# Kernel tuning notes

Hardware: AMD Instinct MI355X
Metric: run time of the kernel (lower is better)

Reference implementation:

```python
import jax, jax.numpy as jnp
import numpy as np
from jax import lax

B, C, H, W = 8, 384, 64, 64


def cos_map(N):
    # ortho DCT-II basis: weight[n, x] = cos(n*(x+0.5)*pi/N) * sqrt(2/N), row 0 /= sqrt(2)
    wx = (jnp.arange(N, dtype=jnp.float32) + 0.5) / N
    wn = jnp.arange(N, dtype=jnp.float32)[:, None]
    w = jnp.cos(wn * wx[None, :] * jnp.pi) * np.sqrt(2.0 / N).astype(np.float32)
    return w.at[0, :].multiply(np.float32(1.0 / np.sqrt(2.0)))


def setup_inputs() -> dict:
    key = jax.random.key(0)
    ks = jax.random.split(key, 8)
    s = 0.05
    return {
        "x": jax.random.normal(ks[0], (B, C, H, W), jnp.float32),
        "freq_embed": jax.random.normal(ks[1], (H, W, C), jnp.float32),
        "dw_w": jax.random.normal(ks[2], (C, 1, 3, 3), jnp.float32) * s,
        "dw_b": jnp.zeros((C,), jnp.float32),
        "lin_w": jax.random.normal(ks[3], (2 * C, C), jnp.float32) * s,
        "lin_b": jnp.zeros((2 * C,), jnp.float32),
        "tok_w": jax.random.normal(ks[4], (C, C), jnp.float32) * s,
        "tok_b": jnp.zeros((C,), jnp.float32),
        "c": jnp.ones((1,), jnp.float32),
        "alpha": jnp.ones((1,), jnp.float32) * 0.1,
        "ln_g": jnp.ones((C,), jnp.float32),
        "ln_b": jnp.zeros((C,), jnp.float32),
        "out_w": jax.random.normal(ks[5], (C, C), jnp.float32) * s,
        "out_b": jnp.zeros((C,), jnp.float32),
    }


def reference(x, freq_embed, dw_w, dw_b, lin_w, lin_b, tok_w, tok_b, c, alpha, ln_g, ln_b, out_w, out_b):
    Bc, Cc, Hc, Wc = x.shape
    # depthwise 3x3 conv
    x = lax.conv_general_dilated(x, dw_w, (1, 1), 'SAME',
                                 feature_group_count=Cc,
                                 dimension_numbers=('NCHW', 'OIHW', 'NCHW'))
    x = x + dw_b[None, :, None, None]
    # linear to 2C (channels-last), split into signal x and gate z
    xz = jnp.einsum('bchw,dc->bhwd', x, lin_w) + lin_b
    xs, z = xz[..., :Cc], xz[..., Cc:]          # [B,H,W,C]
    xs = jnp.transpose(xs, (0, 3, 1, 2))        # [B,C,H,W]
    # 2D ortho DCT-II: D = Wh @ x @ Ww^T
    Wh, Ww = cos_map(Hc), cos_map(Wc)
    Xd = jnp.einsum('nh,bchw,kw->bcnk', Wh, xs, Ww)
    # learned frequency gating: t = ReLU(Linear(freq_embed)), per (H,W,C)
    t = jax.nn.relu(jnp.einsum('hwc,dc->hwd', freq_embed, tok_w) + tok_b)
    ct = jnp.transpose(jnp.cos(c * t), (2, 0, 1))[None]        # [1,C,H,W]
    st = jnp.transpose(jnp.sin(c * t), (2, 0, 1))[None] / c[0]
    # x_u0 == x_v0 == Xd in the original (dct2d applied twice to same x)
    final = ct * Xd + st * (Xd + 0.5 * alpha[0] * Xd)
    # 2D inverse DCT: x = Wh^T @ D @ Ww
    xi = jnp.einsum('nh,bcnk,kw->bchw', Wh, final, Ww)
    # LayerNorm over channels, gate with SiLU(z), output linear
    y = jnp.transpose(xi, (0, 2, 3, 1))          # [B,H,W,C]
    mu = jnp.mean(y, axis=-1, keepdims=True)
    var = jnp.mean((y - mu) ** 2, axis=-1, keepdims=True)
    y = (y - mu) * lax.rsqrt(var + 1e-5) * ln_g + ln_b
    y = y * jax.nn.silu(z)
    y = jnp.einsum('bhwc,dc->bhwd', y, out_w) + out_b
    return jnp.transpose(y, (0, 3, 1, 2))        # [B,C,H,W]
```

## Files before the change

### kernel.cpp

```cpp
#include <hip/hip_runtime.h>

typedef _Float16 h2 __attribute__((ext_vector_type(2)));
typedef _Float16 h4 __attribute__((ext_vector_type(4)));
typedef _Float16 h8 __attribute__((ext_vector_type(8)));
typedef float    f4 __attribute__((ext_vector_type(4)));

#define MFMA32(a,b,c) __builtin_amdgcn_mfma_f32_16x16x32_f16((a),(b),(c),0,0,0)
#define MFMA16(a,b,c) __builtin_amdgcn_mfma_f32_16x16x16f16((a),(b),(c),0,0,0)

#define B_N 8
#define C_N 384
#define P_N 4096
#define PI_F 3.14159265358979323846f

__device__ __forceinline__ h4 to_h4(f4 v) {
  h4 r; r[0]=(_Float16)v[0]; r[1]=(_Float16)v[1]; r[2]=(_Float16)v[2]; r[3]=(_Float16)v[3];
  return r;
}

__device__ __forceinline__ void gl_lds16(const _Float16* g, _Float16* l) {
  __builtin_amdgcn_global_load_lds(
      (const __attribute__((address_space(1))) void*)g,
      (__attribute__((address_space(3))) void*)l, 16, 0, 0);
}

__global__ __launch_bounds__(256) void k_setup(
    const float* __restrict__ lin_w, const float* __restrict__ tok_w,
    const float* __restrict__ out_w, _Float16* __restrict__ lwh,
    _Float16* __restrict__ twh, _Float16* __restrict__ owh,
    _Float16* __restrict__ wmg, _Float16* __restrict__ wmtg) {
  int t = blockIdx.x * 256 + threadIdx.x;
  if (t < 768*384) lwh[t] = (_Float16)lin_w[t];
  if (t < 384*384) { twh[t] = (_Float16)tok_w[t]; owh[t] = (_Float16)out_w[t]; }
  if (t < 4096) {
    int n = t >> 6, h = t & 63;
    float v = cosf((float)n * ((float)h + 0.5f) * (PI_F / 64.0f)) * 0.1767766952966369f;
    if (n == 0) v *= 0.7071067811865476f;
    wmg[n*64 + h]  = (_Float16)v;
    wmtg[h*64 + n] = (_Float16)v;
  }
}

__global__ __launch_bounds__(256) void k_dwconv(
    const float* __restrict__ x, const float* __restrict__ dww,
    const float* __restrict__ dwb, _Float16* __restrict__ xdw) {
  int blk = blockIdx.x;
  int h = blk & 63;
  int rest = blk >> 6;
  int cgi = rest % 6;
  int b = rest / 6;
  int c0 = cgi * 64;
  int t = threadIdx.x;
  int w = t & 63, ci = t >> 6;
  __shared__ _Float16 buf[64 * 68];
  const float* xb = x + (size_t)b * C_N * P_N;
  int wl = (w > 0)  ? w - 1 : 0;
  int wr = (w < 63) ? w + 1 : 63;
  #pragma unroll
  for (int j = 0; j < 8; j++) {
    int lc = ci * 16 + j * 2;
    h2 pr;
    #pragma unroll
    for (int e = 0; e < 2; e++) {
      int c = c0 + lc + e;
      const float* xc = xb + (size_t)c * P_N;
      float k0=dww[c*9+0],k1=dww[c*9+1],k2=dww[c*9+2];
      float k3=dww[c*9+3],k4=dww[c*9+4],k5=dww[c*9+5];
      float k6=dww[c*9+6],k7=dww[c*9+7],k8=dww[c*9+8];
      float top = (h > 0)  ? xc[(h-1)*64 + w] : 0.0f;
      float mid = xc[h*64 + w];
      float bot = (h < 63) ? xc[(h+1)*64 + w] : 0.0f;
      float tl = __shfl(top, wl, 64), tr = __shfl(top, wr, 64);
      float ml = __shfl(mid, wl, 64), mr = __shfl(mid, wr, 64);
      float bl = __shfl(bot, wl, 64), br = __shfl(bot, wr, 64);
      if (w == 0)  { tl = 0.f; ml = 0.f; bl = 0.f; }
      if (w == 63) { tr = 0.f; mr = 0.f; br = 0.f; }
      float acc = dwb[c];
      acc += k0*tl + k1*top + k2*tr;
      acc += k3*ml + k4*mid + k5*mr;
      acc += k6*bl + k7*bot + k8*br;
      pr[e] = (_Float16)acc;
    }
    *(h2*)&buf[w*68 + lc] = pr;
  }
  __syncthreads();
  _Float16* op = xdw + ((size_t)b*P_N + h*64) * C_N + c0;
  #pragma unroll
  for (int i = 0; i < 4; i++) {
    int flat = (t + 256*i) * 4;
    int pix = flat >> 6, cl = flat & 63;
    *(h4*)&op[(size_t)pix*C_N + cl] = *(const h4*)&buf[pix*68 + cl];
  }
}

__global__ __launch_bounds__(256) void k_gate(
    const float* __restrict__ fe, const _Float16* __restrict__ twh,
    const float* __restrict__ tkb, const float* __restrict__ cc,
    const float* __restrict__ aa, _Float16* __restrict__ g) {
  int pt = blockIdx.x & 63, dt = blockIdx.x >> 6;
  int p0 = pt*64, d0 = dt*64;
  int t = threadIdx.x, lane = t & 63, wave = t >> 6;
  int quad = lane >> 4, l15 = lane & 15;
  int wm_ = wave >> 1, wn = wave & 1;
  __shared__ _Float16 la[64*40], lb[64*40];
  int srow = t >> 2, scg = (t & 3) * 8;
  f4 acc[2][2] = {};
  for (int kc = 0; kc < 384; kc += 32) {
    const float* src = fe + (size_t)(p0 + srow)*384 + kc + scg;
    f4 v0 = *(const f4*)src;
    f4 v1 = *(const f4*)(src + 4);
    h8 hv;
    hv[0]=(_Float16)v0[0]; hv[1]=(_Float16)v0[1]; hv[2]=(_Float16)v0[2]; hv[3]=(_Float16)v0[3];
    hv[4]=(_Float16)v1[0]; hv[5]=(_Float16)v1[1]; hv[6]=(_Float16)v1[2]; hv[7]=(_Float16)v1[3];
    *(h8*)&la[srow*40 + scg] = hv;
    *(h8*)&lb[srow*40 + scg] = *(const h8*)&twh[(size_t)(d0 + srow)*384 + kc + scg];
    __syncthreads();
    h8 a0 = *(const h8*)&la[(wm_*32 + l15)*40 + quad*8];
    h8 a1 = *(const h8*)&la[(wm_*32 + 16 + l15)*40 + quad*8];
    h8 b0 = *(const h8*)&lb[(wn*32 + l15)*40 + quad*8];
    h8 b1 = *(const h8*)&lb[(wn*32 + 16 + l15)*40 + quad*8];
    acc[0][0] = MFMA32(a0, b0, acc[0][0]);
    acc[0][1] = MFMA32(a0, b1, acc[0][1]);
    acc[1][0] = MFMA32(a1, b0, acc[1][0]);
    acc[1][1] = MFMA32(a1, b1, acc[1][1]);
    __syncthreads();
  }
  float c0 = cc[0];
  float s1 = (1.0f + 0.5f*aa[0]) / c0;
  #pragma unroll
  for (int i = 0; i < 2; i++)
  #pragma unroll
  for (int j = 0; j < 2; j++) {
    int d  = d0 + wn*32 + j*16 + l15;
    int pl = wm_*32 + i*16 + quad*4;
    float bias = tkb[d];
    h4 hv;
    #pragma unroll
    for (int r = 0; r < 4; r++) {
      float tv = fmaxf(acc[i][j][r] + bias, 0.0f);
      hv[r] = (_Float16)(__cosf(c0*tv) + s1*__sinf(c0*tv));
    }
    *(h4*)&g[(size_t)d*P_N + p0 + pl] = hv;
  }
}

__global__ __launch_bounds__(256) void k_gemm1(
    const _Float16* __restrict__ xdw, const _Float16* __restrict__ lwh,
    const float* __restrict__ lnb, _Float16* __restrict__ xs,
    _Float16* __restrict__ zs) {
  int pt = blockIdx.x & 31;
  int rest = blockIdx.x >> 5;
  int dt = rest % 6, b = rest / 6;
  int p0 = pt * 128, d0 = dt * 128;
  int t = threadIdx.x, lane = t & 63, wave = t >> 6;
  int quad = lane >> 4, l15 = lane & 15;
  int wm = wave >> 1, wn = wave & 1;
  __shared__ _Float16 la[128 * 32];
  __shared__ _Float16 lb[128 * 32];
  int s_row = lane >> 2;
  int s_col = (lane & 3) * 8;
  const _Float16* ga = xdw + ((size_t)b*P_N + p0) * 384 + s_col;
  const _Float16* gb = lwh + (size_t)d0 * 384 + s_col;
  f4 acc[4][4] = {};
  for (int kc = 0; kc < 384; kc += 32) {
    #pragma unroll
    for (int s = 0; s < 2; s++) {
      int seg = wave * 2 + s;
      int row = seg * 16 + s_row;
      gl_lds16(ga + (size_t)row*384 + kc, &la[seg*512 + lane*8]);
      gl_lds16(gb + (size_t)row*384 + kc, &lb[seg*512 + lane*8]);
    }
    __syncthreads();
    h8 af[4], bf[4];
    #pragma unroll
    for (int i = 0; i < 4; i++) {
      af[i] = *(const h8*)&la[(wm*64 + i*16 + l15)*32 + quad*8];
      bf[i] = *(const h8*)&lb[(wn*64 + i*16 + l15)*32 + quad*8];
    }
    #pragma unroll
    for (int i = 0; i < 4; i++)
    #pragma unroll
    for (int j = 0; j < 4; j++)
      acc[i][j] = MFMA32(af[i], bf[j], acc[i][j]);
    __syncthreads();
  }
  bool isz = (d0 >= 384);
  #pragma unroll
  for (int j = 0; j < 4; j++) {
    int d = d0 + wn*64 + j*16 + l15;
    float bias = lnb[d];
    _Float16* dst = isz ? (zs + ((size_t)b*C_N + (d-384)) * P_N)
                        : (xs + ((size_t)b*C_N + d) * P_N);
    #pragma unroll
    for (int i = 0; i < 4; i++) {
      int p = p0 + wm*64 + i*16 + quad*4;
      h4 hv;
      if (isz) {
        #pragma unroll
        for (int r = 0; r < 4; r++) {
          float v = acc[i][j][r] + bias;
          v = v / (1.0f + __expf(-v));
          hv[r] = (_Float16)v;
        }
      } else {
        #pragma unroll
        for (int r = 0; r < 4; r++) hv[r] = (_Float16)(acc[i][j][r] + bias);
      }
      *(h4*)&dst[p] = hv;
    }
  }
}

__global__ __launch_bounds__(256) void k_dct(
    const _Float16* __restrict__ xs, const _Float16* __restrict__ g,
    const _Float16* __restrict__ wmg, const _Float16* __restrict__ wmtg,
    _Float16* __restrict__ xi) {
  int b = blockIdx.x / 96, cg = blockIdx.x % 96;
  int c0 = cg * 4;
  int t = threadIdx.x, wave = t >> 6, lane = t & 63;
  int quad = lane >> 4, l15 = lane & 15;
  __shared__ _Float16 wm_s[64*72];
  __shared__ _Float16 wmt_s[64*72];
  __shared__ _Float16 pb[4][64*72];
  for (int i = t; i < 512; i += 256) {
    int row = i >> 3, col = (i & 7) * 8;
    *(h8*)&wm_s[row*72 + col]  = *(const h8*)&wmg[row*64 + col];
    *(h8*)&wmt_s[row*72 + col] = *(const h8*)&wmtg[row*64 + col];
  }
  const _Float16* xsb = xs + ((size_t)b*C_N + c0) * P_N;
  for (int i = t; i < 2048; i += 256) {
    int pl = i >> 9, idx = i & 511;
    int p = idx * 8, hh = p >> 6, ww = p & 63;
    *(h8*)&pb[pl][hh*72 + ww] = *(const h8*)&xsb[(size_t)pl*P_N + p];
  }
  __syncthreads();
  h8 aS[4][2], bW[4][2];
  #pragma unroll
  for (int I = 0; I < 4; I++)
  #pragma unroll
  for (int kk = 0; kk < 2; kk++) {
    aS[I][kk] = *(const h8*)&pb[wave][(I*16 + l15)*72 + kk*32 + quad*8];
    bW[I][kk] = *(const h8*)&wm_s[(I*16 + l15)*72 + kk*32 + quad*8];
  }
  h4 t1h[4][4];
  #pragma unroll
  for (int I = 0; I < 4; I++)
  #pragma unroll
  for (int J = 0; J < 4; J++) {
    f4 a = {};
    a = MFMA32(aS[I][0], bW[J][0], a);
    a = MFMA32(aS[I][1], bW[J][1], a);
    t1h[I][J] = to_h4(a);
  }
  __syncthreads();
  const _Float16* gb = g + (size_t)c0 * P_N;
  for (int i = t; i < 2048; i += 256) {
    int pl = i >> 9, idx = i & 511;
    int p = idx * 8, hh = p >> 6, ww = p & 63;
    *(h8*)&pb[pl][hh*72 + ww] = *(const h8*)&gb[(size_t)pl*P_N + p];
  }
  __syncthreads();
  f4 t2[4][4] = {};
  #pragma unroll
  for (int I = 0; I < 4; I++)
  #pragma unroll
  for (int K4 = 0; K4 < 4; K4++) {
    h4 af = *(const h4*)&wm_s[(I*16 + l15)*72 + K4*16 + quad*4];
    #pragma unroll
    for (int J = 0; J < 4; J++) t2[I][J] = MFMA16(af, t1h[K4][J], t2[I][J]);
  }
  h4 fh[4][4];
  #pragma unroll
  for (int I = 0; I < 4; I++)
  #pragma unroll
  for (int J = 0; J < 4; J++) {
    int n0 = I*16 + quad*4, k = J*16 + l15;
    h4 r;
    #pragma unroll
    for (int rr = 0; rr < 4; rr++) {
      float gv = (float)pb[wave][(n0+rr)*72 + k];
      r[rr] = (_Float16)(t2[I][J][rr] * gv);
    }
    fh[I][J] = r;
  }
  f4 t3[4][4] = {};
  #pragma unroll
  for (int J = 0; J < 4; J++)
  #pragma unroll
  for (int K4 = 0; K4 < 4; K4++) {
    h4 bf = *(const h4*)&wmt_s[(J*16 + l15)*72 + K4*16 + quad*4];
    #pragma unroll
    for (int I = 0; I < 4; I++) t3[I][J] = MFMA16(fh[K4][I], bf, t3[I][J]);
  }
  h4 t3h[4][4];
  #pragma unroll
  for (int I = 0; I < 4; I++)
  #pragma unroll
  for (int J = 0; J < 4; J++) t3h[I][J] = to_h4(t3[I][J]);
  f4 t4[4][4] = {};
  #pragma unroll
  for (int I = 0; I < 4; I++)
  #pragma unroll
  for (int K4 = 0; K4 < 4; K4++) {
    h4 af = *(const h4*)&wmt_s[(I*16 + l15)*72 + K4*16 + quad*4];
    #pragma unroll
    for (int J = 0; J < 4; J++) t4[I][J] = MFMA16(af, t3h[K4][J], t4[I][J]);
  }
  #pragma unroll
  for (int I = 0; I < 4; I++)
  #pragma unroll
  for (int J = 0; J < 4; J++) {
    int w0 = I*16 + quad*4, hq = J*16 + l15;
    *(h4*)&pb[wave][hq*72 + w0] = to_h4(t4[I][J]);
  }
  __syncthreads();
  _Float16* xib = xi + ((size_t)b*C_N + c0) * P_N;
  for (int i = t; i < 2048; i += 256) {
    int pl = i >> 9, idx = i & 511;
    int p = idx * 8, hh = p >> 6, ww = p & 63;
    *(h8*)&xib[(size_t)pl*P_N + p] = *(const h8*)&pb[pl][hh*72 + ww];
  }
}

__global__ __launch_bounds__(256) void k_stats(
    const _Float16* __restrict__ xi, float* __restrict__ mu, float* __restrict__ rs) {
  int t = threadIdx.x;
  int pl = t & 63, seg = t >> 6;
  int gp = blockIdx.x * 64 + pl;
  int b = gp >> 12, p = gp & 4095;
  const _Float16* base = xi + (size_t)b * C_N * P_N + p;
  float s = 0.f, ss = 0.f;
  for (int c = seg*96; c < seg*96 + 96; c++) {
    float v = (float)base[(size_t)c * P_N];
    s += v; ss += v*v;
  }
  __shared__ float sb[2][4][64];
  sb[0][seg][pl] = s; sb[1][seg][pl] = ss;
  __syncthreads();
  if (seg == 0) {
    float st  = sb[0][0][pl]+sb[0][1][pl]+sb[0][2][pl]+sb[0][3][pl];
    float sst = sb[1][0][pl]+sb[1][1][pl]+sb[1][2][pl]+sb[1][3][pl];
    float m = st * (1.f/384.f);
    float var = sst * (1.f/384.f) - m*m;
    mu[gp] = m;
    rs[gp] = rsqrtf(var + 1e-5f);
  }
}

__global__ __launch_bounds__(256) void k_gemm2(
    const _Float16* __restrict__ xi, const _Float16* __restrict__ zs,
    const _Float16* __restrict__ owh, const float* __restrict__ mu,
    const float* __restrict__ rs, const float* __restrict__ lng,
    const float* __restrict__ lnbv, const float* __restrict__ ob,
    float* __restrict__ out) {
  int pt = blockIdx.x & 31;
  int rest = blockIdx.x >> 5;
  int dt = rest % 3, b = rest / 3;
  int p0 = pt * 128, d0 = dt * 128;
  int t = threadIdx.x, lane = t & 63, wave = t >> 6;
  int quad = lane >> 4, l15 = lane & 15;
  int wm = wave >> 1, wn = wave & 1;
  __shared__ _Float16 la[128 * 40];
  __shared__ _Float16 lb[128 * 32];
  int s_row = lane >> 2, s_col = (lane & 3) * 8;
  const _Float16* gbp = owh + (size_t)d0 * 384 + s_col;
  int pg = t >> 3;
  int cgI = t & 7;
  int pth = p0 + pg * 4;
  f4 muv = *(const f4*)&mu[(size_t)b*P_N + pth];
  f4 rsv = *(const f4*)&rs[(size_t)b*P_N + pth];
  f4 acc[4][4] = {};
  for (int kc = 0; kc < 384; kc += 32) {
    #pragma unroll
    for (int s = 0; s < 2; s++) {
      int seg = wave * 2 + s;
      int row = seg * 16 + s_row;
      gl_lds16(gbp + (size_t)row*384 + kc, &lb[seg*512 + lane*8]);
    }
    int c = kc + cgI * 4;
    f4 gv = *(const f4*)&lng[c];
    f4 bv = *(const f4*)&lnbv[c];
    _Float16 uv[4][4];
    #pragma unroll
    for (int e = 0; e < 4; e++) {
      const _Float16* xp = &xi[((size_t)b*C_N + c + e) * P_N + pth];
      const _Float16* zp = &zs[((size_t)b*C_N + c + e) * P_N + pth];
      h4 xv = *(const h4*)xp;
      h4 zv = *(const h4*)zp;
      #pragma unroll
      for (int q = 0; q < 4; q++) {
        float y = ((float)xv[q] - muv[q]) * rsv[q] * gv[e] + bv[e];
        uv[q][e] = (_Float16)(y * (float)zv[q]);
      }
    }
    #pragma unroll
    for (int q = 0; q < 4; q++) {
      h4 hv; hv[0]=uv[q][0]; hv[1]=uv[q][1]; hv[2]=uv[q][2]; hv[3]=uv[q][3];
      *(h4*)&la[(pg*4 + q)*40 + cgI*4] = hv;
    }
    __syncthreads();
    h8 af[4], bf[4];
    #pragma unroll
    for (int i = 0; i < 4; i++) {
      af[i] = *(const h8*)&la[(wm*64 + i*16 + l15)*40 + quad*8];
      bf[i] = *(const h8*)&lb[(wn*64 + i*16 + l15)*32 + quad*8];
    }
    #pragma unroll
    for (int i = 0; i < 4; i++)
    #pragma unroll
    for (int j = 0; j < 4; j++)
      acc[i][j] = MFMA32(af[i], bf[j], acc[i][j]);
    __syncthreads();
  }
  #pragma unroll
  for (int j = 0; j < 4; j++) {
    int d = d0 + wn*64 + j*16 + l15;
    float bias = ob[d];
    #pragma unroll
    for (int i = 0; i < 4; i++) {
      int p = p0 + wm*64 + i*16 + quad*4;
      f4 v;
      #pragma unroll
      for (int r = 0; r < 4; r++) v[r] = acc[i][j][r] + bias;
      *(f4*)&out[((size_t)b*C_N + d)*P_N + p] = v;
    }
  }
}

extern "C" void kernel_launch(void* const* d_in, const int* in_sizes, int n_in,
                              void* d_out, int out_size, void* d_ws, size_t ws_size,
                              hipStream_t stream) {
  (void)in_sizes; (void)n_in; (void)out_size; (void)ws_size;
  const float* x    = (const float*)d_in[0];
  const float* fe   = (const float*)d_in[1];
  const float* dww  = (const float*)d_in[2];
  const float* dwb  = (const float*)d_in[3];
  const float* linw = (const float*)d_in[4];
  const float* linb = (const float*)d_in[5];
  const float* tokw = (const float*)d_in[6];
  const float* tokb = (const float*)d_in[7];
  const float* cc   = (const float*)d_in[8];
  const float* aa   = (const float*)d_in[9];
  const float* lng  = (const float*)d_in[10];
  const float* lnbv = (const float*)d_in[11];
  const float* outw = (const float*)d_in[12];
  const float* outb = (const float*)d_in[13];
  float* out = (float*)d_out;

  char* ws = (char*)d_ws;
  size_t off = 0;
  auto alloc = [&](size_t bytes) -> void* {
    void* p = ws + off;
    off += (bytes + 255) & ~(size_t)255;
    return p;
  };
  _Float16* lwh  = (_Float16*)alloc((size_t)768*384*2);
  _Float16* twh  = (_Float16*)alloc((size_t)384*384*2);
  _Float16* owh  = (_Float16*)alloc((size_t)384*384*2);
  _Float16* wmg  = (_Float16*)alloc((size_t)64*64*2);
  _Float16* wmtg = (_Float16*)alloc((size_t)64*64*2);
  _Float16* xdw  = (_Float16*)alloc((size_t)B_N*P_N*C_N*2);
  _Float16* xs   = (_Float16*)alloc((size_t)B_N*C_N*P_N*2);
  _Float16* zs   = (_Float16*)alloc((size_t)B_N*C_N*P_N*2);
  _Float16* gg   = (_Float16*)alloc((size_t)C_N*P_N*2);
  float*    mu   = (float*)alloc((size_t)B_N*P_N*4);
  float*    rsd  = (float*)alloc((size_t)B_N*P_N*4);
  _Float16* xi   = xdw;

  k_setup<<<1152, 256, 0, stream>>>(linw, tokw, outw, lwh, twh, owh, wmg, wmtg);
  k_dwconv<<<3072, 256, 0, stream>>>(x, dww, dwb, xdw);
  k_gate<<<384, 256, 0, stream>>>(fe, twh, tokb, cc, aa, gg);
  k_gemm1<<<1536, 256, 0, stream>>>(xdw, lwh, linb, xs, zs);
  k_dct<<<768, 256, 0, stream>>>(xs, gg, wmg, wmtg, xi);
  k_stats<<<512, 256, 0, stream>>>(xi, mu, rsd);
  k_gemm2<<<768, 256, 0, stream>>>(xi, zs, owh, mu, rsd, lng, lnbv, outb, out);
}
```

Baseline: 274.0 us.

## Materialize normalized gated activations channels-last before output GEMM

Replaces the stats kernel with a kernel that transposes xi through shared memory, computes the LayerNorm statistics, applies the norm and SiLU gate, and writes a channels-last fp16 tensor u. The output GEMM then loads both operands with direct global-to-LDS loads instead of doing strided per-channel loads and elementwise work inside its K loop. This removes the recomputation of the normalization across the three d-tiles and the uncoalesced A-operand loads. In exchange it adds an extra full write and read of a B*P*C fp16 tensor and a bank-conflict-prone transpose in LDS.

```diff
diff --git a/kernel.cpp b/kernel.cpp
--- a/kernel.cpp
+++ b/kernel.cpp
@@ -322,37 +322,71 @@
   }
 }
 
-__global__ __launch_bounds__(256) void k_stats(
-    const _Float16* __restrict__ xi, float* __restrict__ mu, float* __restrict__ rs) {
+__global__ __launch_bounds__(256) void k_ubuild(
+    const _Float16* __restrict__ xi, const _Float16* __restrict__ zs,
+    const float* __restrict__ lng, const float* __restrict__ lnbv,
+    _Float16* __restrict__ u) {
+  int b = blockIdx.x >> 6, pt = blockIdx.x & 63;
+  int p0 = pt * 64;
   int t = threadIdx.x;
-  int pl = t & 63, seg = t >> 6;
-  int gp = blockIdx.x * 64 + pl;
-  int b = gp >> 12, p = gp & 4095;
-  const _Float16* base = xi + (size_t)b * C_N * P_N + p;
+  __shared__ _Float16 ut[64 * 392];
+  __shared__ float red[4][64], red2[4][64];
+  __shared__ float muL[64], rsL[64];
+  int cr = t >> 3;
+  int px0 = (t & 7) * 8;
+  const _Float16* xib = xi + (size_t)b * C_N * P_N;
+  #pragma unroll
+  for (int i = 0; i < 12; i++) {
+    int c = cr + 32 * i;
+    h8 v = *(const h8*)&xib[(size_t)c * P_N + p0 + px0];
+    #pragma unroll
+    for (int e = 0; e < 8; e++) ut[(px0 + e) * 392 + c] = v[e];
+  }
+  __syncthreads();
+  int px = t & 63, seg = t >> 6;
   float s = 0.f, ss = 0.f;
-  for (int c = seg*96; c < seg*96 + 96; c++) {
-    float v = (float)base[(size_t)c * P_N];
-    s += v; ss += v*v;
-  }
-  __shared__ float sb[2][4][64];
-  sb[0][seg][pl] = s; sb[1][seg][pl] = ss;
-  __syncthreads();
-  if (seg == 0) {
-    float st  = sb[0][0][pl]+sb[0][1][pl]+sb[0][2][pl]+sb[0][3][pl];
-    float sst = sb[1][0][pl]+sb[1][1][pl]+sb[1][2][pl]+sb[1][3][pl];
+  #pragma unroll
+  for (int j = 0; j < 12; j++) {
+    h8 v = *(const h8*)&ut[px * 392 + seg * 96 + j * 8];
+    #pragma unroll
+    for (int e = 0; e < 8; e++) { float f = (float)v[e]; s += f; ss += f * f; }
+  }
+  red[seg][px] = s; red2[seg][px] = ss;
+  __syncthreads();
+  if (t < 64) {
+    float st  = red[0][t] + red[1][t] + red[2][t] + red[3][t];
+    float sst = red2[0][t] + red2[1][t] + red2[2][t] + red2[3][t];
     float m = st * (1.f/384.f);
-    float var = sst * (1.f/384.f) - m*m;
-    mu[gp] = m;
-    rs[gp] = rsqrtf(var + 1e-5f);
+    float var = sst * (1.f/384.f) - m * m;
+    muL[t] = m; rsL[t] = rsqrtf(var + 1e-5f);
+  }
+  __syncthreads();
+  const _Float16* zb = zs + (size_t)b * C_N * P_N;
+  #pragma unroll
+  for (int i = 0; i < 12; i++) {
+    int c = cr + 32 * i;
+    float g = lng[c], bb = lnbv[c];
+    h8 zv = *(const h8*)&zb[(size_t)c * P_N + p0 + px0];
+    #pragma unroll
+    for (int e = 0; e < 8; e++) {
+      int p = px0 + e;
+      float y = ((float)ut[p * 392 + c] - muL[p]) * rsL[p] * g + bb;
+      ut[p * 392 + c] = (_Float16)(y * (float)zv[e]);
+    }
+  }
+  __syncthreads();
+  _Float16* ub = u + ((size_t)b * P_N + p0) * C_N;
+  #pragma unroll
+  for (int i = 0; i < 12; i++) {
+    int idx = t + 256 * i;
+    int row = idx / 48, ch = idx % 48;
+    *(h8*)&ub[(size_t)row * C_N + ch * 8] = *(const h8*)&ut[row * 392 + ch * 8];
   }
 }
 
 __global__ __launch_bounds__(256) void k_gemm2(
-    const _Float16* __restrict__ xi, const _Float16* __restrict__ zs,
-    const _Float16* __restrict__ owh, const float* __restrict__ mu,
-    const float* __restrict__ rs, const float* __restrict__ lng,
-    const float* __restrict__ lnbv, const float* __restrict__ ob,
-    float* __restrict__ out) {
+    const _Float16* __restrict__ u, const _Float16* __restrict__ owh,
+    const float* __restrict__ ob, float* __restrict__ out) {
   int pt = blockIdx.x & 31;
   int rest = blockIdx.x >> 5;
   int dt = rest % 3, b = rest / 3;
@@ -360,49 +394,26 @@
   int t = threadIdx.x, lane = t & 63, wave = t >> 6;
   int quad = lane >> 4, l15 = lane & 15;
   int wm = wave >> 1, wn = wave & 1;
-  __shared__ _Float16 la[128 * 40];
+  __shared__ _Float16 la[128 * 32];
   __shared__ _Float16 lb[128 * 32];
-  int s_row = lane >> 2, s_col = (lane & 3) * 8;
-  const _Float16* gbp = owh + (size_t)d0 * 384 + s_col;
-  int pg = t >> 3;
-  int cgI = t & 7;
-  int pth = p0 + pg * 4;
-  f4 muv = *(const f4*)&mu[(size_t)b*P_N + pth];
-  f4 rsv = *(const f4*)&rs[(size_t)b*P_N + pth];
+  int s_row = lane >> 2;
+  int s_col = (lane & 3) * 8;
+  const _Float16* ga = u   + ((size_t)b*P_N + p0) * 384 + s_col;
+  const _Float16* gb = owh + (size_t)d0 * 384 + s_col;
   f4 acc[4][4] = {};
   for (int kc = 0; kc < 384; kc += 32) {
     #pragma unroll
     for (int s = 0; s < 2; s++) {
       int seg = wave * 2 + s;
       int row = seg * 16 + s_row;
-      gl_lds16(gbp + (size_t)row*384 + kc, &lb[seg*512 + lane*8]);
-    }
-    int c = kc + cgI * 4;
-    f4 gv = *(const f4*)&lng[c];
-    f4 bv = *(const f4*)&lnbv[c];
-    _Float16 uv[4][4];
-    #pragma unroll
-    for (int e = 0; e < 4; e++) {
-      const _Float16* xp = &xi[((size_t)b*C_N + c + e) * P_N + pth];
-      const _Float16* zp = &zs[((size_t)b*C_N + c + e) * P_N + pth];
-      h4 xv = *(const h4*)xp;
-      h4 zv = *(const h4*)zp;
-      #pragma unroll
-      for (int q = 0; q < 4; q++) {
-        float y = ((float)xv[q] - muv[q]) * rsv[q] * gv[e] + bv[e];
-        uv[q][e] = (_Float16)(y * (float)zv[q]);
-      }
-    }
-    #pragma unroll
-    for (int q = 0; q < 4; q++) {
-      h4 hv; hv[0]=uv[q][0]; hv[1]=uv[q][1]; hv[2]=uv[q][2]; hv[3]=uv[q][3];
-      *(h4*)&la[(pg*4 + q)*40 + cgI*4] = hv;
+      gl_lds16(ga + (size_t)row*384 + kc, &la[seg*512 + lane*8]);
+      gl_lds16(gb + (size_t)row*384 + kc, &lb[seg*512 + lane*8]);
     }
     __syncthreads();
     h8 af[4], bf[4];
     #pragma unroll
     for (int i = 0; i < 4; i++) {
-      af[i] = *(const h8*)&la[(wm*64 + i*16 + l15)*40 + quad*8];
+      af[i] = *(const h8*)&la[(wm*64 + i*16 + l15)*32 + quad*8];
       bf[i] = *(const h8*)&lb[(wn*64 + i*16 + l15)*32 + quad*8];
     }
     #pragma unroll
@@ -463,15 +474,14 @@
   _Float16* xs   = (_Float16*)alloc((size_t)B_N*C_N*P_N*2);
   _Float16* zs   = (_Float16*)alloc((size_t)B_N*C_N*P_N*2);
   _Float16* gg   = (_Float16*)alloc((size_t)C_N*P_N*2);
-  float*    mu   = (float*)alloc((size_t)B_N*P_N*4);
-  float*    rsd  = (float*)alloc((size_t)B_N*P_N*4);
   _Float16* xi   = xdw;
+  _Float16* uu   = xs;
 
   k_setup<<<1152, 256, 0, stream>>>(linw, tokw, outw, lwh, twh, owh, wmg, wmtg);
   k_dwconv<<<3072, 256, 0, stream>>>(x, dww, dwb, xdw);
   k_gate<<<384, 256, 0, stream>>>(fe, twh, tokb, cc, aa, gg);
   k_gemm1<<<1536, 256, 0, stream>>>(xdw, lwh, linb, xs, zs);
   k_dct<<<768, 256, 0, stream>>>(xs, gg, wmg, wmtg, xi);
-  k_stats<<<512, 256, 0, stream>>>(xi, mu, rsd);
-  k_gemm2<<<768, 256, 0, stream>>>(xi, zs, owh, mu, rsd, lng, lnbv, outb, out);
-}
+  k_ubuild<<<512, 256, 0, stream>>>(xi, zs, lng, lnbv, uu);
+  k_gemm2<<<768, 256, 0, stream>>>(uu, owh, outb, out);
+}
```

After: 257.9 us. -5.9%, faster.
